# Kernel tuning notes

Hardware: AMD Instinct MI355X
Metric: run time of the kernel (lower is better)

The kernel has to match this reference:

```python
import jax, jax.numpy as jnp
import numpy as np

B, T, H = 16, 64, 256  # batch, timesteps (= num stacked layers), hidden
L = T                  # MultiRNNCell([cell]*timesteps): layers == timesteps, shared weights


def setup_inputs() -> dict:
    key = jax.random.key(0)
    k1, k2, k3 = jax.random.split(key, 3)
    x = jax.random.normal(k1, (B, T, H), dtype=jnp.float32)
    init_state = jax.random.normal(k2, (L, 2, B, H), dtype=jnp.float32) * 0.1  # [L, (c,h), B, H]
    W = jax.random.normal(k3, (2 * H, 4 * H), dtype=jnp.float32) / np.sqrt(2 * H)
    b = jnp.zeros((4 * H,), dtype=jnp.float32)
    return {"x": x, "init_state": init_state, "W": W, "b": b}


def reference(x, init_state, W, b):
    # TF LSTMCell math: gates order (i, j, f, o), forget_bias = 1.0
    c0 = init_state[:, 0]  # [L,B,H]
    h0 = init_state[:, 1]  # [L,B,H]

    def layer_fn(inp, st):
        # inp: [B,H] input to this layer; st = (c,h) each [B,H]
        lc, lh = st
        z = jnp.concatenate([inp, lh], axis=-1) @ W + b  # [B,4H]
        i, j, f, o = jnp.split(z, 4, axis=-1)
        nc = jax.nn.sigmoid(f + 1.0) * lc + jax.nn.sigmoid(i) * jnp.tanh(j)
        nh = jax.nn.sigmoid(o) * jnp.tanh(nc)
        return nh, (nc, nh)  # carry = input to next layer; ys = new per-layer state

    def step(carry, xt):
        # carry: (c,h) each [L,B,H]; xt: [B,H]
        c, h = carry
        top_h, (nc, nh) = jax.lax.scan(layer_fn, xt, (c, h))
        return (nc, nh), top_h

    (_, _), ys = jax.lax.scan(step, (c0, h0), jnp.transpose(x, (1, 0, 2)))  # ys: [T,B,H]
    return jnp.transpose(ys, (1, 0, 2))  # [B,T,H] top-layer outputs (dynamic_rnn outputs)
```

## Files before the change

kernel.cpp:

```cpp
#include <hip/hip_runtime.h>

typedef _Float16 half8 __attribute__((ext_vector_type(8)));
typedef float f32x4 __attribute__((ext_vector_type(4)));
typedef unsigned int u32x4 __attribute__((ext_vector_type(4)));

#define SC_AGENT __HIP_MEMORY_SCOPE_AGENT

constexpr size_t OFF_PROG = 0;
constexpr size_t OFF_H    = 65536;
constexpr size_t SLOT_STRIDE = (size_t)64 * 16 * 128;

__device__ __forceinline__ size_t Widx(int l, int b, int wi) {
  return ((size_t)l * 16 + b) * 128 + wi;
}
__device__ __forceinline__ float sigm(float v) { return 1.0f / (1.0f + __expf(-v)); }
__device__ __forceinline__ float tanh_(float v) { return 1.0f - 2.0f / (__expf(2.0f * v) + 1.0f); }

#define POLL_LD(dst, base, OFS)                                              \
  asm volatile("global_load_dwordx2 %0, %1, off offset:" #OFS " sc0 sc1"     \
               : "=v"(dst) : "v"(base))

__global__ void init_ws(const float* __restrict__ init_state, char* ws) {
  int* prog = (int*)(ws + OFF_PROG);
  unsigned long long* Hw = (unsigned long long*)(ws + OFF_H);
  const int tid = blockIdx.x * 256 + threadIdx.x;
  if (tid < 256) prog[tid] = -1;
  for (int e = tid; e < 64 * 16 * 128; e += 65536) {
    const int wi = e & 127, b = (e >> 7) & 15, l = e >> 11;
    Hw[Widx(l, b, wi)] = 0xFFFE00000000ULL;
    union { _Float16 f; unsigned short s; } h0, h1;
    h0.f = (_Float16)init_state[((l * 2 + 1) * 16 + b) * 256 + 2 * wi];
    h1.f = (_Float16)init_state[((l * 2 + 1) * 16 + b) * 256 + 2 * wi + 1];
    Hw[SLOT_STRIDE + Widx(l, b, wi)] =
        (unsigned long long)h0.s | ((unsigned long long)h1.s << 16) | (0xFFFFULL << 32);
  }
}

__global__ __launch_bounds__(256, 1) void lstm_mfma(
    const float* __restrict__ x, const float* __restrict__ init_state,
    const float* __restrict__ W, const float* __restrict__ bias,
    float* __restrict__ out, char* ws) {
  int* prog = (int*)(ws + OFF_PROG);
  unsigned long long* Hw = (unsigned long long*)(ws + OFF_H);

  const int tid = threadIdx.x;
  const int wg = blockIdx.x;
  const int l = wg >> 2, r = wg & 3;
  const int wv = tid >> 6, lane = tid & 63;

  __shared__ alignas(16) _Float16 aLds[16 * 64 * 8];
  __shared__ alignas(16) float zLds[16 * 260];
  __shared__ unsigned short hLds[16 * 64];

  half8 wreg[64];
#pragma unroll
  for (int q = 0; q < 4; ++q) {
    const int nl = (wv * 4 + q) * 16 + (lane & 15);
    const int col = (nl & 3) * 256 + r * 64 + (nl >> 2);
#pragma unroll
    for (int kb = 0; kb < 16; ++kb) {
      const int k0 = kb * 32 + (lane >> 4) * 8;
      const float* src = W + (size_t)k0 * 1024 + col;
      half8 hv;
#pragma unroll
      for (int jj = 0; jj < 8; ++jj) hv[jj] = (_Float16)src[(size_t)jj * 1024];
      wreg[q * 16 + kb] = hv;
    }
  }

  const int hu = tid & 63, b4 = tid >> 6;
  const int gu = r * 64 + hu;
  float creg[4];
#pragma unroll
  for (int bb = 0; bb < 4; ++bb)
    creg[bb] = init_state[((l * 2 + 0) * 16 + (b4 * 4 + bb)) * 256 + gu];
  const float bi_ = bias[0 * 256 + gu], bj_ = bias[1 * 256 + gu];
  const float bf_ = bias[2 * 256 + gu], bo_ = bias[3 * 256 + gu];

  int kbA[4], lnA[4];
  size_t wbase[4];
#pragma unroll
  for (int i = 0; i < 4; ++i) {
    const int e = i * 256 + tid, kb = e >> 6, ln = e & 63;
    const int m = ln & 15, k0 = kb * 32 + (ln >> 4) * 8;
    kbA[i] = kb; lnA[i] = ln;
    wbase[i] = (i < 2) ? (l > 0 ? Widx(l - 1, m, k0 >> 1) : 0)
                       : Widx(l, m, (k0 - 256) >> 1);
  }

  int* const progIn = (l > 0) ? &prog[(l - 1) * 4 + r] : prog;
  int* const bpBase = (l < 63) ? &prog[(l + 1) * 4] : prog;

  for (int t = 0; t < 64; ++t) {
    const int slotCur = t & 1, slotPrev = (t + 1) & 1;
    const unsigned expIn = (unsigned)(unsigned short)t;
    const unsigned expOwn = (unsigned)(unsigned short)(t - 1);

    if (l == 0) {
#pragma unroll
      for (int i = 0; i < 2; ++i) {
        const int kb = kbA[i], ln = lnA[i];
        const int m = ln & 15, k0 = kb * 32 + (ln >> 4) * 8;
        const float* xs = x + ((size_t)m * 64 + t) * 256 + k0;
        half8 hv;
#pragma unroll
        for (int jj = 0; jj < 8; ++jj) hv[jj] = (_Float16)xs[jj];
        *(half8*)&aLds[(size_t)(kb * 64 + ln) * 8] = hv;
      }
    }

    if (l > 0) {
      int pl = __hip_atomic_load(progIn, __ATOMIC_RELAXED, SC_AGENT);
      int g = 0;
      while (pl < t - 1) {
        __builtin_amdgcn_s_sleep(8);
        pl = __hip_atomic_load(progIn, __ATOMIC_RELAXED, SC_AGENT);
        if (++g > 400000) break;
      }
    }

    if (tid == 0 && l < 63 && t >= 2) {
      const int need = t - 2;
      int g = 0;
      while (true) {
        u32x4 pv;
        asm volatile("global_load_dwordx4 %0, %1, off sc0 sc1" : "=v"(pv) : "v"(bpBase));
        asm volatile("s_waitcnt vmcnt(0)" ::: "memory");
        __builtin_amdgcn_sched_barrier(0);
        if ((int)pv[0] >= need && (int)pv[1] >= need &&
            (int)pv[2] >= need && (int)pv[3] >= need) break;
        __builtin_amdgcn_s_sleep(2);
        if (++g > 400000) break;
      }
    }

    unsigned pend = (l == 0) ? 0xFF00u : 0xFFFFu;
    int round = 0;
    while (pend) {
      unsigned long long wv_[16];
      const unsigned long long* sp0 = Hw + (slotCur ? SLOT_STRIDE : 0) + wbase[0];
      const unsigned long long* sp1 = Hw + (slotCur ? SLOT_STRIDE : 0) + wbase[1];
      const unsigned long long* sp2 = Hw + (slotPrev ? SLOT_STRIDE : 0) + wbase[2];
      const unsigned long long* sp3 = Hw + (slotPrev ? SLOT_STRIDE : 0) + wbase[3];
      if (pend & 0x0001u) POLL_LD(wv_[0],  sp0, 0);
      if (pend & 0x0002u) POLL_LD(wv_[1],  sp0, 8);
      if (pend & 0x0004u) POLL_LD(wv_[2],  sp0, 16);
      if (pend & 0x0008u) POLL_LD(wv_[3],  sp0, 24);
      if (pend & 0x0010u) POLL_LD(wv_[4],  sp1, 0);
      if (pend & 0x0020u) POLL_LD(wv_[5],  sp1, 8);
      if (pend & 0x0040u) POLL_LD(wv_[6],  sp1, 16);
      if (pend & 0x0080u) POLL_LD(wv_[7],  sp1, 24);
      if (pend & 0x0100u) POLL_LD(wv_[8],  sp2, 0);
      if (pend & 0x0200u) POLL_LD(wv_[9],  sp2, 8);
      if (pend & 0x0400u) POLL_LD(wv_[10], sp2, 16);
      if (pend & 0x0800u) POLL_LD(wv_[11], sp2, 24);
      if (pend & 0x1000u) POLL_LD(wv_[12], sp3, 0);
      if (pend & 0x2000u) POLL_LD(wv_[13], sp3, 8);
      if (pend & 0x4000u) POLL_LD(wv_[14], sp3, 16);
      if (pend & 0x8000u) POLL_LD(wv_[15], sp3, 24);
      asm volatile("s_waitcnt vmcnt(0)" ::: "memory");
      __builtin_amdgcn_sched_barrier(0);
#pragma unroll
      for (int i = 0; i < 4; ++i) {
        unsigned* dp = (unsigned*)&aLds[(size_t)(kbA[i] * 64 + lnA[i]) * 8];
        const unsigned exp_ = (i < 2) ? expIn : expOwn;
#pragma unroll
        for (int j = 0; j < 4; ++j) {
          const int b_ = i * 4 + j;
          if ((pend >> b_) & 1u) {
            const unsigned long long wd = wv_[b_];
            if ((unsigned)(wd >> 32) == exp_) {
              dp[j] = (unsigned)wd;
              pend &= ~(1u << b_);
            }
          }
        }
      }
      if (pend) {
        if (++round > 500000) break;
        if ((round & 15) == 0) __builtin_amdgcn_s_sleep(1);
      }
    }
    __syncthreads();
    if (tid == 0) __hip_atomic_store(&prog[l * 4 + r], t, __ATOMIC_RELAXED, SC_AGENT);

    f32x4 acc[4] = {{0.f, 0.f, 0.f, 0.f}, {0.f, 0.f, 0.f, 0.f},
                    {0.f, 0.f, 0.f, 0.f}, {0.f, 0.f, 0.f, 0.f}};
#pragma unroll
    for (int kb = 0; kb < 16; ++kb) {
      half8 a = *(const half8*)&aLds[(kb * 64 + lane) * 8];
#pragma unroll
      for (int q = 0; q < 4; ++q)
        acc[q] = __builtin_amdgcn_mfma_f32_16x16x32_f16(a, wreg[q * 16 + kb], acc[q], 0, 0, 0);
    }

#pragma unroll
    for (int q = 0; q < 4; ++q) {
      const int nl = (wv * 4 + q) * 16 + (lane & 15);
      const int m0 = (lane >> 4) * 4;
#pragma unroll
      for (int rg = 0; rg < 4; ++rg) zLds[(m0 + rg) * 260 + nl] = acc[q][rg];
    }
    __syncthreads();

#pragma unroll
    for (int bb = 0; bb < 4; ++bb) {
      const int b = b4 * 4 + bb;
      f32x4 zg = *(const f32x4*)&zLds[b * 260 + hu * 4];
      const float iv = zg[0] + bi_, jv = zg[1] + bj_;
      const float fv = zg[2] + bf_, ov = zg[3] + bo_;
      const float nc = sigm(fv + 1.0f) * creg[bb] + sigm(iv) * tanh_(jv);
      const float nh = sigm(ov) * tanh_(nc);
      creg[bb] = nc;
      union { _Float16 f; unsigned short s; } cv;
      cv.f = (_Float16)nh;
      hLds[b * 64 + hu] = cv.s;
      if (l == 63) out[((size_t)b * 64 + t) * 256 + gu] = nh;
    }
    __syncthreads();

    {
      const int b = tid >> 4, lw0 = (tid & 15) * 2;
#pragma unroll
      for (int q = 0; q < 2; ++q) {
        const int lw = lw0 + q, u0 = 2 * lw;
        unsigned lo = (unsigned)hLds[b * 64 + u0] | ((unsigned)hLds[b * 64 + u0 + 1] << 16);
        unsigned long long wd =
            (unsigned long long)lo | ((unsigned long long)expIn << 32);
        __hip_atomic_store(Hw + (slotCur ? SLOT_STRIDE : 0) + Widx(l, b, r * 32 + lw),
                           wd, __ATOMIC_RELAXED, SC_AGENT);
      }
    }
  }
}

extern "C" void kernel_launch(void* const* d_in, const int* in_sizes, int n_in,
                              void* d_out, int out_size, void* d_ws,
                              size_t ws_size, hipStream_t stream) {
  const float* x          = (const float*)d_in[0];
  const float* init_state = (const float*)d_in[1];
  const float* W          = (const float*)d_in[2];
  const float* bias       = (const float*)d_in[3];
  float* out = (float*)d_out;
  char* ws   = (char*)d_ws;

  init_ws<<<256, 256, 0, stream>>>(init_state, ws);
  lstm_mfma<<<256, 256, 0, stream>>>(x, init_state, W, bias, out, ws);
}
```

Baseline: 767.5 us.

## Rework cross-workgroup sync: epoch tags, XCD-aware layer mapping, L2-first polling

Removes the separate progress-counter wait on the upstream layer and relies only on tagged h-words. The tags now carry a per-launch epoch, so stale values from earlier runs cannot match. Workgroups are remapped so that neighbouring layers sit on the same XCD, which lets polls mostly use L2-scoped loads, with a periodic system-coherent load as a fallback. Producer stores are issued twice, once plain and once with sc0 sc1. The backpressure wait is moved before the barrier so it overlaps the gate math. The aim is lower handoff latency along the layer pipeline. The risk is depending on the XCD placement of workgroups for the L2-scoped polls to see fresh data, plus extra store traffic.

```diff
diff --git a/kernel.cpp b/kernel.cpp
--- a/kernel.cpp
+++ b/kernel.cpp
@@ -6,8 +6,9 @@
 
 #define SC_AGENT __HIP_MEMORY_SCOPE_AGENT
 
-constexpr size_t OFF_PROG = 0;
-constexpr size_t OFF_H    = 65536;
+constexpr size_t OFF_PROG  = 0;
+constexpr size_t OFF_EPOCH = 4096;
+constexpr size_t OFF_H     = 65536;
 constexpr size_t SLOT_STRIDE = (size_t)64 * 16 * 128;
 
 __device__ __forceinline__ size_t Widx(int l, int b, int wi) {
@@ -16,23 +17,53 @@
 __device__ __forceinline__ float sigm(float v) { return 1.0f / (1.0f + __expf(-v)); }
 __device__ __forceinline__ float tanh_(float v) { return 1.0f - 2.0f / (__expf(2.0f * v) + 1.0f); }
 
-#define POLL_LD(dst, base, OFS)                                              \
-  asm volatile("global_load_dwordx2 %0, %1, off offset:" #OFS " sc0 sc1"     \
+#define POLL_L2(dst, base, OFS)                                          \
+  asm volatile("global_load_dwordx2 %0, %1, off offset:" #OFS " sc0"     \
                : "=v"(dst) : "v"(base))
+#define POLL_IC(dst, base, OFS)                                          \
+  asm volatile("global_load_dwordx2 %0, %1, off offset:" #OFS " sc0 sc1" \
+               : "=v"(dst) : "v"(base))
+
+#define ISSUE_ALL(M)                          \
+  if (pend & 0x0001u) M(wv_[0],  sp0, 0);     \
+  if (pend & 0x0002u) M(wv_[1],  sp0, 8);     \
+  if (pend & 0x0004u) M(wv_[2],  sp0, 16);    \
+  if (pend & 0x0008u) M(wv_[3],  sp0, 24);    \
+  if (pend & 0x0010u) M(wv_[4],  sp1, 0);     \
+  if (pend & 0x0020u) M(wv_[5],  sp1, 8);     \
+  if (pend & 0x0040u) M(wv_[6],  sp1, 16);    \
+  if (pend & 0x0080u) M(wv_[7],  sp1, 24);    \
+  if (pend & 0x0100u) M(wv_[8],  sp2, 0);     \
+  if (pend & 0x0200u) M(wv_[9],  sp2, 8);     \
+  if (pend & 0x0400u) M(wv_[10], sp2, 16);    \
+  if (pend & 0x0800u) M(wv_[11], sp2, 24);    \
+  if (pend & 0x1000u) M(wv_[12], sp3, 0);     \
+  if (pend & 0x2000u) M(wv_[13], sp3, 8);     \
+  if (pend & 0x4000u) M(wv_[14], sp3, 16);    \
+  if (pend & 0x8000u) M(wv_[15], sp3, 24);
+
+__global__ void bump_epoch(char* ws) {
+  unsigned* ep = (unsigned*)(ws + OFF_EPOCH);
+  unsigned v = __hip_atomic_load(ep, __ATOMIC_RELAXED, SC_AGENT);
+  __hip_atomic_store(ep, v + 1, __ATOMIC_RELAXED, SC_AGENT);
+}
 
 __global__ void init_ws(const float* __restrict__ init_state, char* ws) {
-  int* prog = (int*)(ws + OFF_PROG);
+  unsigned* prog = (unsigned*)(ws + OFF_PROG);
   unsigned long long* Hw = (unsigned long long*)(ws + OFF_H);
+  const unsigned ep = __hip_atomic_load((unsigned*)(ws + OFF_EPOCH),
+                                        __ATOMIC_RELAXED, SC_AGENT);
+  const unsigned long long tagInit = ((unsigned long long)((ep << 8) | 0xFFu)) << 32;
   const int tid = blockIdx.x * 256 + threadIdx.x;
-  if (tid < 256) prog[tid] = -1;
+  if (tid < 256) prog[tid] = (ep << 8) - 1u;
   for (int e = tid; e < 64 * 16 * 128; e += 65536) {
     const int wi = e & 127, b = (e >> 7) & 15, l = e >> 11;
-    Hw[Widx(l, b, wi)] = 0xFFFE00000000ULL;
+    Hw[Widx(l, b, wi)] = 0ULL;
     union { _Float16 f; unsigned short s; } h0, h1;
     h0.f = (_Float16)init_state[((l * 2 + 1) * 16 + b) * 256 + 2 * wi];
     h1.f = (_Float16)init_state[((l * 2 + 1) * 16 + b) * 256 + 2 * wi + 1];
     Hw[SLOT_STRIDE + Widx(l, b, wi)] =
-        (unsigned long long)h0.s | ((unsigned long long)h1.s << 16) | (0xFFFFULL << 32);
+        (unsigned long long)h0.s | ((unsigned long long)h1.s << 16) | tagInit;
   }
 }
 
@@ -40,13 +71,17 @@
     const float* __restrict__ x, const float* __restrict__ init_state,
     const float* __restrict__ W, const float* __restrict__ bias,
     float* __restrict__ out, char* ws) {
-  int* prog = (int*)(ws + OFF_PROG);
+  unsigned* prog = (unsigned*)(ws + OFF_PROG);
   unsigned long long* Hw = (unsigned long long*)(ws + OFF_H);
 
   const int tid = threadIdx.x;
   const int wg = blockIdx.x;
-  const int l = wg >> 2, r = wg & 3;
+  const int l = ((wg & 7) << 3) | (wg >> 5);
+  const int r = (wg >> 3) & 3;
   const int wv = tid >> 6, lane = tid & 63;
+
+  const unsigned epb = __hip_atomic_load((unsigned*)(ws + OFF_EPOCH),
+                                         __ATOMIC_RELAXED, SC_AGENT) << 8;
 
   __shared__ alignas(16) _Float16 aLds[16 * 64 * 8];
   __shared__ alignas(16) float zLds[16 * 260];
@@ -88,13 +123,12 @@
                        : Widx(l, m, (k0 - 256) >> 1);
   }
 
-  int* const progIn = (l > 0) ? &prog[(l - 1) * 4 + r] : prog;
-  int* const bpBase = (l < 63) ? &prog[(l + 1) * 4] : prog;
+  unsigned* const bpBase = (l < 63) ? &prog[(l + 1) * 4] : prog;
 
   for (int t = 0; t < 64; ++t) {
     const int slotCur = t & 1, slotPrev = (t + 1) & 1;
-    const unsigned expIn = (unsigned)(unsigned short)t;
-    const unsigned expOwn = (unsigned)(unsigned short)(t - 1);
+    const unsigned expIn = epb | (unsigned)t;
+    const unsigned expOwn = (t > 0) ? (epb | (unsigned)(t - 1)) : (epb | 0xFFu);
 
     if (l == 0) {
 #pragma unroll
@@ -106,31 +140,6 @@
 #pragma unroll
         for (int jj = 0; jj < 8; ++jj) hv[jj] = (_Float16)xs[jj];
         *(half8*)&aLds[(size_t)(kb * 64 + ln) * 8] = hv;
-      }
-    }
-
-    if (l > 0) {
-      int pl = __hip_atomic_load(progIn, __ATOMIC_RELAXED, SC_AGENT);
-      int g = 0;
-      while (pl < t - 1) {
-        __builtin_amdgcn_s_sleep(8);
-        pl = __hip_atomic_load(progIn, __ATOMIC_RELAXED, SC_AGENT);
-        if (++g > 400000) break;
-      }
-    }
-
-    if (tid == 0 && l < 63 && t >= 2) {
-      const int need = t - 2;
-      int g = 0;
-      while (true) {
-        u32x4 pv;
-        asm volatile("global_load_dwordx4 %0, %1, off sc0 sc1" : "=v"(pv) : "v"(bpBase));
-        asm volatile("s_waitcnt vmcnt(0)" ::: "memory");
-        __builtin_amdgcn_sched_barrier(0);
-        if ((int)pv[0] >= need && (int)pv[1] >= need &&
-            (int)pv[2] >= need && (int)pv[3] >= need) break;
-        __builtin_amdgcn_s_sleep(2);
-        if (++g > 400000) break;
       }
     }
 
@@ -142,22 +151,7 @@
       const unsigned long long* sp1 = Hw + (slotCur ? SLOT_STRIDE : 0) + wbase[1];
       const unsigned long long* sp2 = Hw + (slotPrev ? SLOT_STRIDE : 0) + wbase[2];
       const unsigned long long* sp3 = Hw + (slotPrev ? SLOT_STRIDE : 0) + wbase[3];
-      if (pend & 0x0001u) POLL_LD(wv_[0],  sp0, 0);
-      if (pend & 0x0002u) POLL_LD(wv_[1],  sp0, 8);
-      if (pend & 0x0004u) POLL_LD(wv_[2],  sp0, 16);
-      if (pend & 0x0008u) POLL_LD(wv_[3],  sp0, 24);
-      if (pend & 0x0010u) POLL_LD(wv_[4],  sp1, 0);
-      if (pend & 0x0020u) POLL_LD(wv_[5],  sp1, 8);
-      if (pend & 0x0040u) POLL_LD(wv_[6],  sp1, 16);
-      if (pend & 0x0080u) POLL_LD(wv_[7],  sp1, 24);
-      if (pend & 0x0100u) POLL_LD(wv_[8],  sp2, 0);
-      if (pend & 0x0200u) POLL_LD(wv_[9],  sp2, 8);
-      if (pend & 0x0400u) POLL_LD(wv_[10], sp2, 16);
-      if (pend & 0x0800u) POLL_LD(wv_[11], sp2, 24);
-      if (pend & 0x1000u) POLL_LD(wv_[12], sp3, 0);
-      if (pend & 0x2000u) POLL_LD(wv_[13], sp3, 8);
-      if (pend & 0x4000u) POLL_LD(wv_[14], sp3, 16);
-      if (pend & 0x8000u) POLL_LD(wv_[15], sp3, 24);
+      if ((round & 3) == 3) { ISSUE_ALL(POLL_IC) } else { ISSUE_ALL(POLL_L2) }
       asm volatile("s_waitcnt vmcnt(0)" ::: "memory");
       __builtin_amdgcn_sched_barrier(0);
 #pragma unroll
@@ -178,11 +172,16 @@
       }
       if (pend) {
         if (++round > 500000) break;
-        if ((round & 15) == 0) __builtin_amdgcn_s_sleep(1);
+        if ((round & 15) == 15) __builtin_amdgcn_s_sleep(1);
       }
     }
     __syncthreads();
-    if (tid == 0) __hip_atomic_store(&prog[l * 4 + r], t, __ATOMIC_RELAXED, SC_AGENT);
+    if (tid == 0) {
+      unsigned pv = epb | (unsigned)t;
+      unsigned* pp = &prog[l * 4 + r];
+      asm volatile("global_store_dword %0, %1, off" :: "v"(pp), "v"(pv) : "memory");
+      asm volatile("global_store_dword %0, %1, off sc0 sc1" :: "v"(pp), "v"(pv) : "memory");
+    }
 
     f32x4 acc[4] = {{0.f, 0.f, 0.f, 0.f}, {0.f, 0.f, 0.f, 0.f},
                     {0.f, 0.f, 0.f, 0.f}, {0.f, 0.f, 0.f, 0.f}};
@@ -217,6 +216,24 @@
       hLds[b * 64 + hu] = cv.s;
       if (l == 63) out[((size_t)b * 64 + t) * 256 + gu] = nh;
     }
+
+    if (tid == 0 && l < 63 && t >= 2) {
+      const unsigned need = epb | (unsigned)(t - 2);
+      int g = 0;
+      while (true) {
+        u32x4 pv;
+        if (g & 1) {
+          asm volatile("global_load_dwordx4 %0, %1, off sc0 sc1" : "=v"(pv) : "v"(bpBase));
+        } else {
+          asm volatile("global_load_dwordx4 %0, %1, off sc0" : "=v"(pv) : "v"(bpBase));
+        }
+        asm volatile("s_waitcnt vmcnt(0)" ::: "memory");
+        __builtin_amdgcn_sched_barrier(0);
+        if (pv[0] >= need && pv[1] >= need && pv[2] >= need && pv[3] >= need) break;
+        __builtin_amdgcn_s_sleep(1);
+        if (++g > 500000) break;
+      }
+    }
     __syncthreads();
 
     {
@@ -227,8 +244,10 @@
         unsigned lo = (unsigned)hLds[b * 64 + u0] | ((unsigned)hLds[b * 64 + u0 + 1] << 16);
         unsigned long long wd =
             (unsigned long long)lo | ((unsigned long long)expIn << 32);
-        __hip_atomic_store(Hw + (slotCur ? SLOT_STRIDE : 0) + Widx(l, b, r * 32 + lw),
-                           wd, __ATOMIC_RELAXED, SC_AGENT);
+        unsigned long long* dst =
+            Hw + (slotCur ? SLOT_STRIDE : 0) + Widx(l, b, r * 32 + lw);
+        asm volatile("global_store_dwordx2 %0, %1, off" :: "v"(dst), "v"(wd) : "memory");
+        asm volatile("global_store_dwordx2 %0, %1, off sc0 sc1" :: "v"(dst), "v"(wd) : "memory");
       }
     }
   }
@@ -244,6 +263,7 @@
   float* out = (float*)d_out;
   char* ws   = (char*)d_ws;
 
+  bump_epoch<<<1, 1, 0, stream>>>(ws);
   init_ws<<<256, 256, 0, stream>>>(init_state, ws);
   lstm_mfma<<<256, 256, 0, stream>>>(x, init_state, W, bias, out, ws);
 }
```

New measurement: 1.191 ms. 1.55x slower.
